# Performance work log

Measured on AMD Instinct MI355X. Metric: run time of the kernel, lower is better.

## Reference

```python
import jax, jax.numpy as jnp
import numpy as np

D = 768          # wav2vec2-base hidden size
H = 4            # cross-attn heads
HD = D // H
B = 8
N = 1024         # w2v sequence length (target length)
T = 2000         # raw CQCC frames
N_GAT = 3
NUM_CLASSES = 2


def _p(key, shape, scale=0.02):
    return jax.random.normal(key, shape, dtype=jnp.float32) * scale


def layer_norm(x, g, b, eps=1e-5):
    m = x.mean(-1, keepdims=True)
    v = x.var(-1, keepdims=True)
    return (x - m) * jax.lax.rsqrt(v + eps) * g + b


def gelu(x):
    return jax.nn.gelu(x, approximate=False)


def conv1d(x, w, b):
    # x [B,C,T], w [O,I,K], padding=1 (same)
    y = jax.lax.conv_general_dilated(x, w, (1,), [(1, 1)], dimension_numbers=('NCH', 'OIH', 'NCH'))
    return y + b[None, :, None]


def batchnorm(x, g, b, m, v, eps=1e-5):
    # eval-mode BatchNorm1d on [B,C,T]
    return (x - m[None, :, None]) * jax.lax.rsqrt(v[None, :, None] + eps) * g[None, :, None] + b[None, :, None]


def interp_linear(x, target_len):
    # torch F.interpolate(mode='linear', align_corners=False); x [B,T,D] -> [B,target_len,D]
    t_in = x.shape[1]
    pos = (jnp.arange(target_len, dtype=jnp.float32) + 0.5) * (t_in / target_len) - 0.5
    pos = jnp.clip(pos, 0.0, t_in - 1.0)
    lo = jnp.floor(pos).astype(jnp.int32)
    hi = jnp.minimum(lo + 1, t_in - 1)
    w = (pos - lo.astype(jnp.float32))[None, :, None]
    return x[:, lo] * (1.0 - w) + x[:, hi] * w


def mha(q, k, v, in_w, in_b, out_w, out_b):
    # torch nn.MultiheadAttention, batch_first=True
    bb, nq, _ = q.shape
    nk = k.shape[1]
    wq, wk, wv = in_w[:D], in_w[D:2 * D], in_w[2 * D:]
    bq, bk, bv = in_b[:D], in_b[D:2 * D], in_b[2 * D:]
    qh = (q @ wq.T + bq).reshape(bb, nq, H, HD).transpose(0, 2, 1, 3)
    kh = (k @ wk.T + bk).reshape(bb, nk, H, HD).transpose(0, 2, 1, 3)
    vh = (v @ wv.T + bv).reshape(bb, nk, H, HD).transpose(0, 2, 1, 3)
    scores = jnp.einsum('bhqd,bhkd->bhqk', qh, kh) * (1.0 / np.sqrt(HD))
    alpha = jax.nn.softmax(scores, axis=-1)
    o = jnp.einsum('bhqk,bhkd->bhqd', alpha, vh).transpose(0, 2, 1, 3).reshape(bb, nq, D)
    return o @ out_w.T + out_b


def graph_attn(x, fc_w, fc_b, a_w, a_b):
    # GAT score on concat([h_i, h_j]) decomposes additively: e_ij = a_i.h_i + a_j.h_j + b
    h = x @ fc_w.T + fc_b                      # [B,N,D]
    s_i = h @ a_w[:D]                          # [B,N]
    s_j = h @ a_w[D:]                          # [B,N]
    e = s_i[:, :, None] + s_j[:, None, :] + a_b  # [B,N,N]
    alpha = jax.nn.softmax(e, axis=-1)
    return jnp.einsum('bij,bjd->bid', alpha, h)


def _forward(w2v, cqcc, conv1_w, conv1_b, bn1_g, bn1_b, bn1_m, bn1_v,
             conv2_w, conv2_b, bn2_g, bn2_b, bn2_m, bn2_v, pos_embed,
             lnq_g, lnq_b, lnkv_g, lnkv_b,
             a1_in_w, a1_in_b, a1_out_w, a1_out_b,
             a2_in_w, a2_in_b, a2_out_w, a2_out_b,
             gat_fc_w, gat_fc_b, gat_a_w, gat_a_b, gln_g, gln_b,
             clf_w1, clf_b1, clf_w2, clf_b2):
    # CQCC conv stack
    x = gelu(batchnorm(conv1d(cqcc, conv1_w, conv1_b), bn1_g, bn1_b, bn1_m, bn1_v))
    x = gelu(batchnorm(conv1d(x, conv2_w, conv2_b), bn2_g, bn2_b, bn2_m, bn2_v))  # [B,D,T]
    cq = interp_linear(x.transpose(0, 2, 1), w2v.shape[1])  # [B,N,D]
    # shared positional encoding
    n = w2v.shape[1]
    w = w2v + pos_embed[:, :n]
    cq = cq + pos_embed[:, :n]
    # bidirectional cross attention (norm_q / norm_kv shared across directions)
    out1 = mha(layer_norm(cq, lnq_g, lnq_b), layer_norm(w, lnkv_g, lnkv_b),
               layer_norm(w, lnkv_g, lnkv_b), a1_in_w, a1_in_b, a1_out_w, a1_out_b)
    out2 = mha(layer_norm(w, lnq_g, lnq_b), layer_norm(cq, lnkv_g, lnkv_b),
               layer_norm(cq, lnkv_g, lnkv_b), a2_in_w, a2_in_b, a2_out_w, a2_out_b)
    x = out1 + out2
    # 3 residual graph-attention blocks
    for l in range(N_GAT):
        res = x
        x = graph_attn(x, gat_fc_w[l], gat_fc_b[l], gat_a_w[l], gat_a_b[l])
        x = layer_norm(x + res, gln_g[l], gln_b[l])
    pooled = x.mean(axis=1)
    h = gelu(pooled @ clf_w1.T + clf_b1)
    return h @ clf_w2.T + clf_b2


def setup_inputs():
    ks = iter(jax.random.split(jax.random.key(0), 64))
    inp = {}
    inp['w2v'] = jax.random.normal(next(ks), (B, N, D), dtype=jnp.float32)
    inp['cqcc'] = jax.random.normal(next(ks), (B, 20, T), dtype=jnp.float32)
    inp['conv1_w'] = _p(next(ks), (128, 20, 3)); inp['conv1_b'] = jnp.zeros((128,), jnp.float32)
    inp['bn1_g'] = jnp.ones((128,), jnp.float32); inp['bn1_b'] = jnp.zeros((128,), jnp.float32)
    inp['bn1_m'] = jnp.zeros((128,), jnp.float32); inp['bn1_v'] = jnp.ones((128,), jnp.float32)
    inp['conv2_w'] = _p(next(ks), (D, 128, 3)); inp['conv2_b'] = jnp.zeros((D,), jnp.float32)
    inp['bn2_g'] = jnp.ones((D,), jnp.float32); inp['bn2_b'] = jnp.zeros((D,), jnp.float32)
    inp['bn2_m'] = jnp.zeros((D,), jnp.float32); inp['bn2_v'] = jnp.ones((D,), jnp.float32)
    inp['pos_embed'] = _p(next(ks), (1, 2000, D), 1.0)
    inp['lnq_g'] = jnp.ones((D,), jnp.float32); inp['lnq_b'] = jnp.zeros((D,), jnp.float32)
    inp['lnkv_g'] = jnp.ones((D,), jnp.float32); inp['lnkv_b'] = jnp.zeros((D,), jnp.float32)
    inp['a1_in_w'] = _p(next(ks), (3 * D, D)); inp['a1_in_b'] = jnp.zeros((3 * D,), jnp.float32)
    inp['a1_out_w'] = _p(next(ks), (D, D)); inp['a1_out_b'] = jnp.zeros((D,), jnp.float32)
    inp['a2_in_w'] = _p(next(ks), (3 * D, D)); inp['a2_in_b'] = jnp.zeros((3 * D,), jnp.float32)
    inp['a2_out_w'] = _p(next(ks), (D, D)); inp['a2_out_b'] = jnp.zeros((D,), jnp.float32)
    inp['gat_fc_w'] = _p(next(ks), (N_GAT, D, D)); inp['gat_fc_b'] = jnp.zeros((N_GAT, D), jnp.float32)
    inp['gat_a_w'] = _p(next(ks), (N_GAT, 2 * D)); inp['gat_a_b'] = jnp.zeros((N_GAT,), jnp.float32)
    inp['gln_g'] = jnp.ones((N_GAT, D), jnp.float32); inp['gln_b'] = jnp.zeros((N_GAT, D), jnp.float32)
    inp['clf_w1'] = _p(next(ks), (128, D)); inp['clf_b1'] = jnp.zeros((128,), jnp.float32)
    inp['clf_w2'] = _p(next(ks), (NUM_CLASSES, 128)); inp['clf_b2'] = jnp.zeros((NUM_CLASSES,), jnp.float32)
    return inp


def reference(w2v, cqcc, conv1_w, conv1_b, bn1_g, bn1_b, bn1_m, bn1_v,
              conv2_w, conv2_b, bn2_g, bn2_b, bn2_m, bn2_v, pos_embed,
              lnq_g, lnq_b, lnkv_g, lnkv_b,
              a1_in_w, a1_in_b, a1_out_w, a1_out_b,
              a2_in_w, a2_in_b, a2_out_w, a2_out_b,
              gat_fc_w, gat_fc_b, gat_a_w, gat_a_b, gln_g, gln_b,
              clf_w1, clf_b1, clf_w2, clf_b2):
    return _forward(w2v, cqcc, conv1_w, conv1_b, bn1_g, bn1_b, bn1_m, bn1_v,
                    conv2_w, conv2_b, bn2_g, bn2_b, bn2_m, bn2_v, pos_embed,
                    lnq_g, lnq_b, lnkv_g, lnkv_b,
                    a1_in_w, a1_in_b, a1_out_w, a1_out_b,
                    a2_in_w, a2_in_b, a2_out_w, a2_out_b,
                    gat_fc_w, gat_fc_b, gat_a_w, gat_a_b, gln_g, gln_b,
                    clf_w1, clf_b1, clf_w2, clf_b2)
```

## Files before the change

kernel.cpp:

```cpp
#include <hip/hip_runtime.h>
#include <math.h>

#define DD 768
#define NH 4
#define HDIM 192
#define BBATCH 8
#define NSEQ 1024
#define TLEN 2000
#define SLOT 6291456
#define XROW 256256

typedef _Float16 h16;
typedef _Float16 half8v __attribute__((ext_vector_type(8)));
typedef _Float16 half4v __attribute__((ext_vector_type(4)));
typedef float f32x4 __attribute__((ext_vector_type(4)));

__device__ __forceinline__ float gelu_f(float x){
  return 0.5f * x * (1.0f + erff(x * 0.70710678118654752440f));
}
__device__ __forceinline__ float wave_sum(float v){
  #pragma unroll
  for (int off = 32; off; off >>= 1) v += __shfl_xor(v, off);
  return v;
}
__device__ __forceinline__ float wave_max(float v){
  #pragma unroll
  for (int off = 32; off; off >>= 1) v = fmaxf(v, __shfl_xor(v, off));
  return v;
}
__device__ __forceinline__ void gload16(const h16* g, h16* l){
  __builtin_amdgcn_global_load_lds(
      (const __attribute__((address_space(1))) void*)g,
      (__attribute__((address_space(3))) void*)l, 16, 0, 0);
}
__device__ __forceinline__ int xcd_remap(int orig, int nwg){
  int q = nwg >> 3, r = nwg & 7;
  int xcd = orig & 7, idx = orig >> 3;
  return (xcd < r ? xcd * (q + 1) : r * (q + 1) + (xcd - r) * q) + idx;
}

struct CastArgs {
  const float* s[5];
  h16* d[5];
  int cum[6];
};
__global__ __launch_bounds__(256) void k_cast5(CastArgs a, int total){
  int i = blockIdx.x * 256 + threadIdx.x;
  if (i >= total) return;
  int seg = 0;
  #pragma unroll
  for (int t = 1; t < 5; ++t) seg += (i >= a.cum[t]);
  int off = i - a.cum[seg];
  a.d[seg][off] = (h16)a.s[seg][off];
}

__global__ __launch_bounds__(256) void k_castc2(const float* __restrict__ s,
    h16* __restrict__ d){
  int i = blockIdx.x * 256 + threadIdx.x;
  if (i >= 294912) return;
  int oc = i / 384, rem = i % 384;
  int ic = rem / 3, kh = rem % 3;
  d[oc * 384 + kh * 128 + ic] = (h16)s[i];
}

__global__ __launch_bounds__(256) void k_conv1t(const float* __restrict__ cqcc,
    const float* __restrict__ w, const float* __restrict__ bias,
    const float* __restrict__ g, const float* __restrict__ be,
    const float* __restrict__ mm, const float* __restrict__ vv,
    h16* __restrict__ X){
  __shared__ float xs[20][258];
  __shared__ float wsm[32*60];
  const int t0 = blockIdx.x * 256;
  const int ocg = blockIdx.y, b = blockIdx.z;
  const int tid = threadIdx.x;
  for (int idx = tid; idx < 20*258; idx += 256){
    int ic = idx / 258, tt = idx % 258;
    int t = t0 + tt - 1;
    xs[ic][tt] = (t >= 0 && t < TLEN) ? cqcc[((size_t)b*20 + ic)*TLEN + t] : 0.f;
  }
  for (int idx = tid; idx < 32*60; idx += 256)
    wsm[idx] = w[ocg*32*60 + idx];
  __syncthreads();
  int t = t0 + tid;
  if (t >= TLEN) return;
  float acc[32] = {};
  for (int ic = 0; ic < 20; ++ic){
    float x0 = xs[ic][tid], x1v = xs[ic][tid+1], x2v = xs[ic][tid+2];
    #pragma unroll
    for (int oc = 0; oc < 32; ++oc){
      const float* wp = &wsm[(oc*20 + ic)*3];
      acc[oc] += wp[0]*x0 + wp[1]*x1v + wp[2]*x2v;
    }
  }
  h16* dst = X + (size_t)b*XROW + (size_t)(t+1)*128 + ocg*32;
  #pragma unroll 4
  for (int oc = 0; oc < 32; ++oc){
    int c = ocg*32 + oc;
    float s = rsqrtf(vv[c] + 1e-5f) * g[c];
    float val = (acc[oc] + bias[c] - mm[c]) * s + be[c];
    dst[oc] = (h16)gelu_f(val);
  }
  if (t == 0){
    h16* z = X + (size_t)b*XROW + ocg*32;
    #pragma unroll
    for (int oc = 0; oc < 32; ++oc) z[oc] = (h16)0.f;
  }
  if (t == TLEN-1){
    h16* z = X + (size_t)b*XROW + (size_t)2001*128 + ocg*32;
    #pragma unroll
    for (int oc = 0; oc < 32; ++oc) z[oc] = (h16)0.f;
  }
}

__global__ void k_bnprep(const float* __restrict__ cb, const float* __restrict__ g,
    const float* __restrict__ be, const float* __restrict__ m,
    const float* __restrict__ v, float* __restrict__ sc, float* __restrict__ off){
  int i = blockIdx.x * 256 + threadIdx.x;
  if (i >= DD) return;
  float s = g[i] * rsqrtf(v[i] + 1e-5f);
  sc[i] = s;
  off[i] = (cb[i] - m[i]) * s + be[i];
}

__global__ __launch_bounds__(256) void k_interp_ln(const h16* __restrict__ x2,
    const float* __restrict__ pe,
    const float* __restrict__ g1, const float* __restrict__ b1, h16* __restrict__ o1,
    const float* __restrict__ g2, const float* __restrict__ b2, h16* __restrict__ o2){
  __shared__ float ss[4], sqq[4];
  int row = blockIdx.x, tid = threadIdx.x;
  int b = row >> 10, i = row & 1023;
  float p = (i + 0.5f) * ((float)TLEN / (float)NSEQ) - 0.5f;
  p = fminf(fmaxf(p, 0.f), (float)(TLEN - 1));
  int lo = (int)floorf(p);
  int hi = min(lo + 1, TLEN - 1);
  float w = p - (float)lo;
  const h16* blo = x2 + ((size_t)b * TLEN + lo) * DD;
  const h16* bhi = x2 + ((size_t)b * TLEN + hi) * DD;
  const float* per = pe + (size_t)i * DD;
  float v[3]; float s = 0.f, sq = 0.f;
  #pragma unroll
  for (int j = 0; j < 3; ++j){
    int d = j * 256 + tid;
    float x = (float)blo[d] * (1.f - w) + (float)bhi[d] * w + per[d];
    v[j] = x; s += x; sq += x * x;
  }
  s = wave_sum(s); sq = wave_sum(sq);
  int wv = tid >> 6;
  if ((tid & 63) == 0){ ss[wv] = s; sqq[wv] = sq; }
  __syncthreads();
  s  = ss[0] + ss[1] + ss[2] + ss[3];
  sq = sqq[0] + sqq[1] + sqq[2] + sqq[3];
  float mean = s * (1.f / DD);
  float var  = sq * (1.f / DD) - mean * mean;
  float r = rsqrtf(var + 1e-5f);
  #pragma unroll
  for (int j = 0; j < 3; ++j){
    int d = j * 256 + tid;
    float xn = (v[j] - mean) * r;
    o1[(size_t)row * DD + d] = (h16)(xn * g1[d] + b1[d]);
    o2[(size_t)row * DD + d] = (h16)(xn * g2[d] + b2[d]);
  }
}

__global__ __launch_bounds__(256) void k_addpos_ln(const float* __restrict__ xin,
    const float* __restrict__ pe,
    const float* __restrict__ g1, const float* __restrict__ b1, h16* __restrict__ o1,
    const float* __restrict__ g2, const float* __restrict__ b2, h16* __restrict__ o2){
  __shared__ float ss[4], sqq[4];
  int row = blockIdx.x, tid = threadIdx.x;
  int i = row & 1023;
  const float* ip = xin + (size_t)row * DD;
  const float* per = pe + (size_t)i * DD;
  float v[3]; float s = 0.f, sq = 0.f;
  #pragma unroll
  for (int j = 0; j < 3; ++j){
    int d = j * 256 + tid;
    float x = ip[d] + per[d];
    v[j] = x; s += x; sq += x * x;
  }
  s = wave_sum(s); sq = wave_sum(sq);
  int wv = tid >> 6;
  if ((tid & 63) == 0){ ss[wv] = s; sqq[wv] = sq; }
  __syncthreads();
  s  = ss[0] + ss[1] + ss[2] + ss[3];
  sq = sqq[0] + sqq[1] + sqq[2] + sqq[3];
  float mean = s * (1.f / DD);
  float var  = sq * (1.f / DD) - mean * mean;
  float r = rsqrtf(var + 1e-5f);
  #pragma unroll
  for (int j = 0; j < 3; ++j){
    int d = j * 256 + tid;
    float xn = (v[j] - mean) * r;
    o1[(size_t)row * DD + d] = (h16)(xn * g1[d] + b1[d]);
    o2[(size_t)row * DD + d] = (h16)(xn * g2[d] + b2[d]);
  }
}

__global__ __launch_bounds__(256) void k_lnH(const h16* __restrict__ in,
    const float* __restrict__ ctx, const float* __restrict__ g,
    const float* __restrict__ be, h16* __restrict__ out){
  __shared__ float ss[4], sqq[4];
  int row = blockIdx.x, tid = threadIdx.x;
  const h16* ip = in + (size_t)row * DD;
  int b = row >> 10;
  float v[3]; float s = 0.f, sq = 0.f;
  #pragma unroll
  for (int j = 0; j < 3; ++j){
    int d = j * 256 + tid;
    float x = (float)ip[d] + ctx[b * DD + d];
    v[j] = x; s += x; sq += x * x;
  }
  s = wave_sum(s); sq = wave_sum(sq);
  int w = tid >> 6;
  if ((tid & 63) == 0){ ss[w] = s; sqq[w] = sq; }
  __syncthreads();
  s  = ss[0] + ss[1] + ss[2] + ss[3];
  sq = sqq[0] + sqq[1] + sqq[2] + sqq[3];
  float mean = s * (1.f / DD);
  float var  = sq * (1.f / DD) - mean * mean;
  float r = rsqrtf(var + 1e-5f);
  #pragma unroll
  for (int j = 0; j < 3; ++j){
    int d = j * 256 + tid;
    out[(size_t)row * DD + d] = (h16)((v[j] - mean) * r * g[d] + be[d]);
  }
}

__global__ __launch_bounds__(256) void k_addh(const h16* __restrict__ a,
    const h16* __restrict__ b, h16* __restrict__ o, int n8){
  int i = blockIdx.x * 256 + threadIdx.x;
  if (i < n8){
    half8v x = ((const half8v*)a)[i];
    half8v y = ((const half8v*)b)[i];
    ((half8v*)o)[i] = x + y;
  }
}

#define GEMM_MAINLOOP(Abase, lda, Wbase, ldw, Kdim)                          \
  auto stage = [&](int buf, int kt){                                         \
    _Pragma("unroll")                                                        \
    for (int i = 0; i < 4; ++i){                                             \
      int p = i*256 + tid; int row = p >> 3; int ch = (p & 7) ^ (row & 7);   \
      gload16(Abase + (size_t)(m0+row)*lda + kt + ch*8, &Als[buf][p*8]);     \
    }                                                                        \
    _Pragma("unroll")                                                        \
    for (int i = 0; i < 4; ++i){                                             \
      int p = i*256 + tid; int row = p >> 3; int ch = (p & 7) ^ (row & 7);   \
      gload16(Wbase + (size_t)(n0+row)*ldw + kt + ch*8, &Bls[buf][p*8]);     \
    }                                                                        \
  };                                                                         \
  stage(0, 0);                                                               \
  const int nk = Kdim >> 6;                                                  \
  for (int t = 0; t < nk; ++t){                                              \
    const int cur = t & 1;                                                   \
    if (t + 1 < nk){                                                         \
      stage(cur ^ 1, (t + 1) << 6);                                          \
      asm volatile("s_waitcnt vmcnt(8)" ::: "memory");                       \
    } else {                                                                 \
      asm volatile("s_waitcnt vmcnt(0)" ::: "memory");                       \
    }                                                                        \
    __builtin_amdgcn_s_barrier();                                            \
    __builtin_amdgcn_sched_barrier(0);                                       \
    __builtin_amdgcn_s_setprio(1);                                           \
    _Pragma("unroll")                                                        \
    for (int kk = 0; kk < 2; ++kk){                                          \
      half8v af[4], bf[4];                                                   \
      _Pragma("unroll")                                                      \
      for (int mi = 0; mi < 4; ++mi){                                        \
        int row = wr*64 + mi*16 + lr;                                        \
        int chp = (kk*4 + lg) ^ (row & 7);                                   \
        af[mi] = *(const half8v*)&Als[cur][row*64 + chp*8];                  \
      }                                                                      \
      _Pragma("unroll")                                                      \
      for (int ni = 0; ni < 4; ++ni){                                        \
        int row = wc*64 + ni*16 + lr;                                        \
        int chp = (kk*4 + lg) ^ (row & 7);                                   \
        bf[ni] = *(const half8v*)&Bls[cur][row*64 + chp*8];                  \
      }                                                                      \
      _Pragma("unroll")                                                      \
      for (int mi = 0; mi < 4; ++mi)                                         \
        _Pragma("unroll")                                                    \
        for (int ni = 0; ni < 4; ++ni)                                       \
          acc[mi][ni] = __builtin_amdgcn_mfma_f32_16x16x32_f16(              \
              af[mi], bf[ni], acc[mi][ni], 0, 0, 0);                         \
    }                                                                        \
    __builtin_amdgcn_s_setprio(0);                                           \
    asm volatile("s_waitcnt lgkmcnt(0)" ::: "memory");                       \
    __builtin_amdgcn_sched_barrier(0);                                       \
    __builtin_amdgcn_s_barrier();                                            \
  }

__global__ __launch_bounds__(256) void k_gemm_h(
    const h16* __restrict__ A, const h16* __restrict__ W,
    int lda, int ldw, int ldc, int K,
    const float* __restrict__ bias,
    h16* __restrict__ outh,
    const float* __restrict__ rdw, float* __restrict__ rdpart)
{
  __shared__ h16 Als[2][128*64];
  __shared__ h16 Bls[2][128*64];
  const int tid = threadIdx.x;
  const int gx = gridDim.x, gy = gridDim.y;
  const int wg = xcd_remap(blockIdx.x + gx * blockIdx.y, gx * gy);
  const int nidx = wg % gx;
  const int n0 = nidx * 128, m0 = (wg / gx) * 128;
  const int lane = tid & 63, wid = tid >> 6;
  const int wr = wid >> 1, wc = wid & 1;
  const int lr = lane & 15, lg = lane >> 4;
  f32x4 acc[4][4] = {};
  GEMM_MAINLOOP(A, lda, W, ldw, K)
  float rd[4][4] = {};
  #pragma unroll
  for (int mi = 0; mi < 4; ++mi){
    #pragma unroll
    for (int ni = 0; ni < 4; ++ni){
      int col = n0 + wc*64 + ni*16 + lr;
      int rowb = m0 + wr*64 + mi*16 + lg*4;
      float cb = bias[col];
      float aw = rdw ? rdw[col] : 0.f;
      #pragma unroll
      for (int r = 0; r < 4; ++r){
        size_t idx = (size_t)(rowb + r) * ldc + col;
        float v = acc[mi][ni][r] + cb;
        outh[idx] = (h16)v;
        if (rdw) rd[mi][r] += v * aw;
      }
    }
  }
  if (rdw){
    #pragma unroll
    for (int mi = 0; mi < 4; ++mi){
      #pragma unroll
      for (int r = 0; r < 4; ++r){
        float p = rd[mi][r];
        #pragma unroll
        for (int o = 1; o < 16; o <<= 1) p += __shfl_xor(p, o);
        if (lr == 0){
          int row = m0 + wr*64 + mi*16 + lg*4 + r;
          rdpart[(size_t)row * 12 + nidx*2 + wc] = p;
        }
      }
    }
  }
}

__global__ __launch_bounds__(256) void k_gemmop(
    const h16* __restrict__ A0, const h16* __restrict__ A1,
    const h16* __restrict__ W0, const h16* __restrict__ W1,
    const float* __restrict__ bb0, const float* __restrict__ bb1,
    h16* __restrict__ C0, h16* __restrict__ C1)
{
  __shared__ h16 Als[2][128*64];
  __shared__ h16 Bls[2][128*64];
  const int tid = threadIdx.x;
  const int gx = gridDim.x, gy = gridDim.y;
  const int nwg = gx * gy * 2;
  const int wg = xcd_remap(blockIdx.x + gx*(blockIdx.y + gy*blockIdx.z), nwg);
  const int n0 = (wg % gx) * 128;
  const int m0 = ((wg / gx) % gy) * 128;
  const int bz = wg / (gx * gy);
  const h16* A = bz ? A1 : A0;
  const h16* W = bz ? W1 : W0;
  const float* bias = bz ? bb1 : bb0;
  h16* C = bz ? C1 : C0;
  const int lane = tid & 63, wid = tid >> 6;
  const int wr = wid >> 1, wc = wid & 1;
  const int lr = lane & 15, lg = lane >> 4;
  f32x4 acc[4][4] = {};
  GEMM_MAINLOOP(A, DD, W, DD, DD)
  #pragma unroll
  for (int mi = 0; mi < 4; ++mi){
    #pragma unroll
    for (int ni = 0; ni < 4; ++ni){
      int col = n0 + wc*64 + ni*16 + lr;
      int rowb = m0 + wr*64 + mi*16 + lg*4;
      float cb = bias[col];
      #pragma unroll
      for (int r = 0; r < 4; ++r)
        C[(size_t)(rowb + r) * DD + col] = (h16)(acc[mi][ni][r] + cb);
    }
  }
}

__global__ __launch_bounds__(256) void k_conv2g(
    const h16* __restrict__ X, const h16* __restrict__ W,
    const float* __restrict__ sc, const float* __restrict__ off,
    h16* __restrict__ out)
{
  __shared__ h16 Als[2][128*64];
  __shared__ h16 Bls[2][128*64];
  const int tid = threadIdx.x;
  const int gx = gridDim.x, gy = gridDim.y;
  const int wg = xcd_remap(blockIdx.x + gx * blockIdx.y, gx * gy);
  const int n0 = (wg % gx) * 128, m0 = (wg / gx) * 128;
  const int lane = tid & 63, wid = tid >> 6;
  const int wr = wid >> 1, wc = wid & 1;
  const int lr = lane & 15, lg = lane >> 4;
  f32x4 acc[4][4] = {};
  auto stage = [&](int buf, int kt){
    #pragma unroll
    for (int i = 0; i < 4; ++i){
      int p = i*256 + tid; int row = p >> 3; int ch = (p & 7) ^ (row & 7);
      int rm = m0 + row, b = rm >> 11, t = rm & 2047;
      gload16(X + (size_t)b*XROW + (size_t)t*128 + kt + ch*8, &Als[buf][p*8]);
    }
    #pragma unroll
    for (int i = 0; i < 4; ++i){
      int p = i*256 + tid; int row = p >> 3; int ch = (p & 7) ^ (row & 7);
      gload16(W + (size_t)(n0+row)*384 + kt + ch*8, &Bls[buf][p*8]);
    }
  };
  stage(0, 0);
  const int nk = 6;
  for (int t = 0; t < nk; ++t){
    const int cur = t & 1;
    if (t + 1 < nk){
      stage(cur ^ 1, (t + 1) << 6);
      asm volatile("s_waitcnt vmcnt(8)" ::: "memory");
    } else {
      asm volatile("s_waitcnt vmcnt(0)" ::: "memory");
    }
    __builtin_amdgcn_s_barrier();
    __builtin_amdgcn_sched_barrier(0);
    __builtin_amdgcn_s_setprio(1);
    #pragma unroll
    for (int kk = 0; kk < 2; ++kk){
      half8v af[4], bf[4];
      #pragma unroll
      for (int mi = 0; mi < 4; ++mi){
        int row = wr*64 + mi*16 + lr;
        int chp = (kk*4 + lg) ^ (row & 7);
        af[mi] = *(const half8v*)&Als[cur][row*64 + chp*8];
      }
      #pragma unroll
      for (int ni = 0; ni < 4; ++ni){
        int row = wc*64 + ni*16 + lr;
        int chp = (kk*4 + lg) ^ (row & 7);
        bf[ni] = *(const half8v*)&Bls[cur][row*64 + chp*8];
      }
      #pragma unroll
      for (int mi = 0; mi < 4; ++mi)
        #pragma unroll
        for (int ni = 0; ni < 4; ++ni)
          acc[mi][ni] = __builtin_amdgcn_mfma_f32_16x16x32_f16(
              af[mi], bf[ni], acc[mi][ni], 0, 0, 0);
    }
    __builtin_amdgcn_s_setprio(0);
    asm volatile("s_waitcnt lgkmcnt(0)" ::: "memory");
    __builtin_amdgcn_sched_barrier(0);
    __builtin_amdgcn_s_barrier();
  }
  #pragma unroll
  for (int mi = 0; mi < 4; ++mi){
    #pragma unroll
    for (int ni = 0; ni < 4; ++ni){
      int col = n0 + wc*64 + ni*16 + lr;
      int rowb = m0 + wr*64 + mi*16 + lg*4;
      #pragma unroll
      for (int r = 0; r < 4; ++r){
        int rm = rowb + r, b = rm >> 11, t = rm & 2047;
        if (t < TLEN){
          float v = acc[mi][ni][r] * sc[col] + off[col];
          out[((size_t)b*TLEN + t)*DD + col] = (h16)gelu_f(v);
        }
      }
    }
  }
}

__global__ __launch_bounds__(256) void k_gemm6(
    const h16* __restrict__ Lall, const h16* __restrict__ w6,
    const float* __restrict__ b1, const float* __restrict__ b2,
    h16* __restrict__ qkv6)
{
  __shared__ h16 Als[2][128*64];
  __shared__ h16 Bls[2][128*64];
  const int tid = threadIdx.x;
  const int gx = gridDim.x, gy = gridDim.y;
  const int nwg = gx * gy * 6;
  const int wg = xcd_remap(blockIdx.x + gx*(blockIdx.y + gy*blockIdx.z), nwg);
  const int n0 = (wg % gx) * 128;
  const int m0 = ((wg / gx) % gy) * 128;
  const int bz = wg / (gx * gy);
  const int aidx = (1468 >> (2*bz)) & 3;
  const h16* A = Lall + (size_t)aidx * SLOT;
  const h16* W = w6 + (size_t)bz * 589824;
  const float* bias = (bz < 3 ? b1 + bz*DD : b2 + (bz-3)*DD);
  h16* C = qkv6 + (size_t)bz * SLOT;
  const int lane = tid & 63, wid = tid >> 6;
  const int wr = wid >> 1, wc = wid & 1;
  const int lr = lane & 15, lg = lane >> 4;
  f32x4 acc[4][4] = {};
  GEMM_MAINLOOP(A, DD, W, DD, DD)
  #pragma unroll
  for (int mi = 0; mi < 4; ++mi){
    #pragma unroll
    for (int ni = 0; ni < 4; ++ni){
      int col = n0 + wc*64 + ni*16 + lr;
      int rowb = m0 + wr*64 + mi*16 + lg*4;
      float cb = bias[col];
      #pragma unroll
      for (int r = 0; r < 4; ++r)
        C[(size_t)(rowb + r) * DD + col] = (h16)(acc[mi][ni][r] + cb);
    }
  }
}

__global__ __launch_bounds__(256) void k_trV(const h16* __restrict__ V0,
    const h16* __restrict__ V1, h16* __restrict__ VT0, h16* __restrict__ VT1){
  __shared__ h16 tile[64*64];
  const int zz = blockIdx.z;
  const int which = zz >> 5, bh = zz & 31;
  const int b = bh >> 2, h = bh & 3;
  const h16* Vh = which ? V1 : V0;
  h16* VT = which ? VT1 : VT0;
  const int q0 = blockIdx.x * 64, d0 = blockIdx.y * 64;
  const int t = threadIdx.x;
  {
    int qq = t >> 2, ds = (t & 3) * 16;
    const h16* src = Vh + ((size_t)b*NSEQ + q0 + qq)*DD + h*HDIM + d0 + ds;
    half8v v0 = *(const half8v*)src;
    half8v v1 = *(const half8v*)(src + 8);
    int c0 = (ds >> 3) ^ (qq & 7), c1 = ((ds >> 3) + 1) ^ (qq & 7);
    *(half8v*)&tile[qq*64 + c0*8] = v0;
    *(half8v*)&tile[qq*64 + c1*8] = v1;
  }
  __syncthreads();
  {
    int dd = t >> 2, qs = (t & 3) * 16;
    half8v o0, o1;
    #pragma unroll
    for (int j = 0; j < 8; ++j){
      int q = qs + j, q2 = qs + 8 + j;
      o0[j] = tile[q*64  + (((dd>>3) ^ (q&7))*8)  + (dd & 7)];
      o1[j] = tile[q2*64 + (((dd>>3) ^ (q2&7))*8) + (dd & 7)];
    }
    h16* dst = VT + (size_t)bh*HDIM*NSEQ + (size_t)(d0+dd)*NSEQ + q0 + qs;
    *(half8v*)dst = o0;
    *(half8v*)(dst + 8) = o1;
  }
}

__global__ __launch_bounds__(256, 3) void k_flash(
    const h16* __restrict__ Q0, const h16* __restrict__ K0,
    const h16* __restrict__ T0, h16* __restrict__ O0,
    const h16* __restrict__ Q1, const h16* __restrict__ K1,
    const h16* __restrict__ T1, h16* __restrict__ O1){
  __shared__ h16 Ks[2][32*192];
  __shared__ h16 Vs[2][192*32];
  __shared__ h16 Ps[4][16*32];
  const int tid = threadIdx.x;
  const int bh = blockIdx.x, qt = blockIdx.y, which = blockIdx.z;
  const int b = bh >> 2, h = bh & 3;
  const int q0 = qt * 64;
  const h16* Qp = which ? Q1 : Q0;
  const h16* Kp = which ? K1 : K0;
  const h16* VTp = which ? T1 : T0;
  h16* Op = which ? O1 : O0;
  const h16* Qg = Qp + (size_t)b*NSEQ*DD + h*HDIM;
  const h16* Kg = Kp + (size_t)b*NSEQ*DD + h*HDIM;
  const h16* Vg = VTp + (size_t)bh*HDIM*NSEQ;
  const int lane = tid & 63, wid = tid >> 6;
  const int lr = lane & 15, lg = lane >> 4;
  const float SC2 = 0.07216878364870322f * 1.4426950408889634f;
  half8v qf[6];
  {
    int qrow = q0 + wid*16 + lr;
    const h16 qs2 = (h16)SC2;
    #pragma unroll
    for (int ks = 0; ks < 6; ++ks){
      half8v qv = *(const half8v*)(Qg + (size_t)qrow*DD + ks*32 + lg*8);
      #pragma unroll
      for (int j = 0; j < 8; ++j) qv[j] = qv[j] * qs2;
      qf[ks] = qv;
    }
  }
  auto stageK = [&](int buf, int k0){
    #pragma unroll
    for (int i = 0; i < 3; ++i){
      int p = i*256 + tid;
      int row = p / 24, chp = p % 24;
      int ch = chp ^ (row & 7);
      gload16(Kg + (size_t)(k0+row)*DD + ch*8, &Ks[buf][p*8]);
    }
  };
  auto stageV = [&](int buf, int k0){
    #pragma unroll
    for (int i = 0; i < 3; ++i){
      int p = i*256 + tid;
      int row = p >> 2, chp = p & 3;
      int ch = chp ^ ((row >> 1) & 3);
      gload16(Vg + (size_t)row*NSEQ + k0 + ch*8, &Vs[buf][p*8]);
    }
  };
  stageK(0, 0); stageV(0, 0);
  f32x4 oacc[12] = {};
  f32x4 osum = {0.f, 0.f, 0.f, 0.f};
  float m2[4] = {-1e30f, -1e30f, -1e30f, -1e30f};
  half8v vone;
  #pragma unroll
  for (int j = 0; j < 8; ++j) vone[j] = (h16)1.f;
  for (int kt = 0; kt < 32; ++kt){
    const int cur = kt & 1;
    if (kt + 1 < 32){
      stageK(cur^1, (kt+1)*32); stageV(cur^1, (kt+1)*32);
      asm volatile("s_waitcnt vmcnt(6)" ::: "memory");
    } else {
      asm volatile("s_waitcnt vmcnt(0)" ::: "memory");
    }
    __builtin_amdgcn_s_barrier();
    __builtin_amdgcn_sched_barrier(0);
    f32x4 sacc[2] = {};
    __builtin_amdgcn_s_setprio(1);
    #pragma unroll
    for (int ks = 0; ks < 6; ++ks){
      #pragma unroll
      for (int t = 0; t < 2; ++t){
        int krow = t*16 + lr;
        int ch = (ks*4 + lg) ^ (krow & 7);
        half8v kf = *(const half8v*)&Ks[cur][krow*192 + ch*8];
        sacc[t] = __builtin_amdgcn_mfma_f32_16x16x32_f16(qf[ks], kf, sacc[t], 0, 0, 0);
      }
    }
    __builtin_amdgcn_s_setprio(0);
    float lmaxr[4];
    #pragma unroll
    for (int r = 0; r < 4; ++r) lmaxr[r] = fmaxf(sacc[0][r], sacc[1][r]);
    bool flag = false;
    #pragma unroll
    for (int r = 0; r < 4; ++r) flag |= (lmaxr[r] > m2[r] + 14.f);
    if (__ballot(flag)){
      float c[4];
      #pragma unroll
      for (int r = 0; r < 4; ++r){
        float mt = lmaxr[r];
        #pragma unroll
        for (int off = 1; off < 16; off <<= 1) mt = fmaxf(mt, __shfl_xor(mt, off));
        if (mt > m2[r]){ c[r] = exp2f(m2[r] - mt); m2[r] = mt; }
        else c[r] = 1.f;
      }
      #pragma unroll
      for (int dt = 0; dt < 12; ++dt){
        f32x4 o = oacc[dt];
        o[0] *= c[0]; o[1] *= c[1]; o[2] *= c[2]; o[3] *= c[3];
        oacc[dt] = o;
      }
      osum[0] *= c[0]; osum[1] *= c[1]; osum[2] *= c[2]; osum[3] *= c[3];
    }
    #pragma unroll
    for (int t = 0; t < 2; ++t){
      #pragma unroll
      for (int r = 0; r < 4; ++r){
        float p = exp2f(sacc[t][r] - m2[r]);
        int q = lg*4 + r, key = t*16 + lr;
        int ch = (t*2 + (lr>>3)) ^ ((q>>1) & 3);
        Ps[wid][q*32 + ch*8 + (key & 7)] = (h16)p;
      }
    }
    asm volatile("s_waitcnt lgkmcnt(0)" ::: "memory");
    __builtin_amdgcn_sched_barrier(0);
    {
      int pch = lg ^ ((lr >> 1) & 3);
      half8v pf = *(const half8v*)&Ps[wid][lr*32 + pch*8];
      __builtin_amdgcn_s_setprio(1);
      #pragma unroll
      for (int dt = 0; dt < 12; ++dt){
        int drow = dt*16 + lr;
        int vch = lg ^ ((drow >> 1) & 3);
        half8v vf = *(const half8v*)&Vs[cur][drow*32 + vch*8];
        oacc[dt] = __builtin_amdgcn_mfma_f32_16x16x32_f16(pf, vf, oacc[dt], 0, 0, 0);
      }
      osum = __builtin_amdgcn_mfma_f32_16x16x32_f16(pf, vone, osum, 0, 0, 0);
      __builtin_amdgcn_s_setprio(0);
    }
    asm volatile("s_waitcnt lgkmcnt(0)" ::: "memory");
    __builtin_amdgcn_sched_barrier(0);
    __builtin_amdgcn_s_barrier();
  }
  float inv[4];
  #pragma unroll
  for (int r = 0; r < 4; ++r) inv[r] = 1.0f / osum[r];
  h16* Og = Op + (size_t)b*NSEQ*DD + h*HDIM;
  #pragma unroll
  for (int dt = 0; dt < 12; ++dt){
    #pragma unroll
    for (int r = 0; r < 4; ++r){
      int q = q0 + wid*16 + lg*4 + r;
      Og[(size_t)q*DD + dt*16 + lr] = (h16)(oacc[dt][r] * inv[r]);
    }
  }
}

__global__ __launch_bounds__(256) void k_ctxs(const float* __restrict__ rdpart,
    const h16* __restrict__ h, float* __restrict__ part){
  __shared__ float red[4];
  __shared__ float al[64];
  const int tid = threadIdx.x;
  const int b = blockIdx.y, pc = blockIdx.z;
  float v[4]; float mx = -1e30f;
  #pragma unroll
  for (int j = 0; j < 4; ++j){
    int i = j * 256 + tid;
    const float* p = rdpart + (size_t)(b * NSEQ + i) * 12;
    float s = 0.f;
    #pragma unroll
    for (int k = 0; k < 12; ++k) s += p[k];
    v[j] = s; mx = fmaxf(mx, s);
  }
  mx = wave_max(mx);
  if ((tid & 63) == 0) red[tid >> 6] = mx;
  __syncthreads();
  mx = fmaxf(fmaxf(red[0], red[1]), fmaxf(red[2], red[3]));
  __syncthreads();
  float s = 0.f;
  #pragma unroll
  for (int j = 0; j < 4; ++j){ v[j] = __expf(v[j] - mx); s += v[j]; }
  s = wave_sum(s);
  if ((tid & 63) == 0) red[tid >> 6] = s;
  __syncthreads();
  s = red[0] + red[1] + red[2] + red[3];
  float inv = 1.0f / s;
  #pragma unroll
  for (int j = 0; j < 4; ++j){
    int i = j * 256 + tid;
    int rel = i - pc * 64;
    if (rel >= 0 && rel < 64) al[rel] = v[j] * inv;
  }
  __syncthreads();
  int d = blockIdx.x * 256 + tid;
  float acc = 0.f;
  const h16* hp = h + ((size_t)b * NSEQ + pc * 64) * DD + d;
  #pragma unroll 4
  for (int j = 0; j < 64; ++j) acc += al[j] * (float)hp[(size_t)j * DD];
  part[(size_t)(b * 16 + pc) * DD + d] = acc;
}

__global__ __launch_bounds__(256) void k_ctx2(const float* __restrict__ part,
    float scale, float* __restrict__ ctx){
  int d = blockIdx.x * 256 + threadIdx.x;
  int b = blockIdx.y;
  if (d >= DD) return;
  float acc = 0.f;
  #pragma unroll
  for (int p = 0; p < 16; ++p) acc += part[(size_t)(b * 16 + p) * DD + d];
  ctx[b * DD + d] = acc * scale;
}

__global__ __launch_bounds__(256) void k_pool1(const h16* __restrict__ x,
    float* __restrict__ part){
  int d = blockIdx.x * 256 + threadIdx.x;
  int b = blockIdx.y, pc = blockIdx.z;
  if (d >= DD) return;
  float acc = 0.f;
  const h16* xp = x + ((size_t)b * NSEQ + pc * 64) * DD + d;
  #pragma unroll 4
  for (int j = 0; j < 64; ++j) acc += (float)xp[(size_t)j * DD];
  part[(size_t)(b * 16 + pc) * DD + d] = acc;
}

__global__ __launch_bounds__(128) void k_clf(const float* __restrict__ pooled,
    const float* __restrict__ w1, const float* __restrict__ b1,
    const float* __restrict__ w2, const float* __restrict__ b2,
    float* __restrict__ out){
  __shared__ float pl[DD];
  __shared__ float h1[128];
  int b = blockIdx.x, tid = threadIdx.x;
  #pragma unroll
  for (int j = 0; j < 6; ++j) pl[j * 128 + tid] = pooled[b * DD + j * 128 + tid];
  __syncthreads();
  float acc = b1[tid];
  const float* wp = w1 + (size_t)tid * DD;
  for (int d = 0; d < DD; ++d) acc += pl[d] * wp[d];
  h1[tid] = gelu_f(acc);
  __syncthreads();
  if (tid < 2){
    float o = b2[tid];
    const float* w2p = w2 + tid * 128;
    for (int c = 0; c < 128; ++c) o += h1[c] * w2p[c];
    out[b * 2 + tid] = o;
  }
}

extern "C" void kernel_launch(void* const* d_in, const int* in_sizes, int n_in,
                              void* d_out, int out_size, void* d_ws, size_t ws_size,
                              hipStream_t stream){
  (void)in_sizes; (void)n_in; (void)out_size;
  const float* w2v      = (const float*)d_in[0];
  const float* cqcc     = (const float*)d_in[1];
  const float* conv1_w  = (const float*)d_in[2];
  const float* conv1_b  = (const float*)d_in[3];
  const float* bn1_g    = (const float*)d_in[4];
  const float* bn1_b    = (const float*)d_in[5];
  const float* bn1_m    = (const float*)d_in[6];
  const float* bn1_v    = (const float*)d_in[7];
  const float* conv2_w  = (const float*)d_in[8];
  const float* conv2_b  = (const float*)d_in[9];
  const float* bn2_g    = (const float*)d_in[10];
  const float* bn2_b    = (const float*)d_in[11];
  const float* bn2_m    = (const float*)d_in[12];
  const float* bn2_v    = (const float*)d_in[13];
  const float* pos_embed= (const float*)d_in[14];
  const float* lnq_g    = (const float*)d_in[15];
  const float* lnq_b    = (const float*)d_in[16];
  const float* lnkv_g   = (const float*)d_in[17];
  const float* lnkv_b   = (const float*)d_in[18];
  const float* a1_in_w  = (const float*)d_in[19];
  const float* a1_in_b  = (const float*)d_in[20];
  const float* a1_out_w = (const float*)d_in[21];
  const float* a1_out_b = (const float*)d_in[22];
  const float* a2_in_w  = (const float*)d_in[23];
  const float* a2_in_b  = (const float*)d_in[24];
  const float* a2_out_w = (const float*)d_in[25];
  const float* a2_out_b = (const float*)d_in[26];
  const float* gat_fc_w = (const float*)d_in[27];
  const float* gat_fc_b = (const float*)d_in[28];
  const float* gat_a_w  = (const float*)d_in[29];
  const float* gln_g    = (const float*)d_in[31];
  const float* gln_b    = (const float*)d_in[32];
  const float* clf_w1   = (const float*)d_in[33];
  const float* clf_b1   = (const float*)d_in[34];
  const float* clf_w2   = (const float*)d_in[35];
  const float* clf_b2   = (const float*)d_in[36];

  char* wsp = (char*)d_ws;
  auto F = [&](size_t bytes){ char* p = wsp; wsp += (bytes + 255) & ~(size_t)255; return p; };
  h16* xh      = (h16*)F(12582912);
  h16* Lall    = (h16*)F(4*12582912);
  h16* qkv6    = (h16*)F(6*12582912);
  h16* VT      = (h16*)F(12582912);
  h16* VT2     = (h16*)F(12582912);
  h16* o1h     = (h16*)F(12582912);
  h16* o2h     = (h16*)F(12582912);
  h16* w6      = (h16*)F(2*3538944);
  h16* w_a1out = (h16*)F(1179648);
  h16* w_a2out = (h16*)F(1179648);
  h16* w_gat   = (h16*)F(3538944);
  h16* w_c2    = (h16*)F(589824);
  float* scb   = (float*)F(3072);
  float* offb  = (float*)F(3072);
  float* ctxb  = (float*)F(24576);
  float* pooled= (float*)F(24576);
  float* partb = (float*)F(393216);
  float* partc = (float*)F(393216);
  if ((size_t)(wsp - (char*)d_ws) > ws_size) return;

  h16* X   = Lall;
  h16* x2h = qkv6;
  h16* hh  = qkv6;

  const int NR = BBATCH * NSEQ;

  {
    CastArgs ca;
    ca.s[0]=a1_in_w;  ca.d[0]=w6;            int n0=1769472;
    ca.s[1]=a2_in_w;  ca.d[1]=w6+1769472;    int n1=1769472;
    ca.s[2]=a1_out_w; ca.d[2]=w_a1out;       int n2=589824;
    ca.s[3]=a2_out_w; ca.d[3]=w_a2out;       int n3=589824;
    ca.s[4]=gat_fc_w; ca.d[4]=w_gat;         int n4=1769472;
    ca.cum[0]=0; ca.cum[1]=n0; ca.cum[2]=n0+n1; ca.cum[3]=n0+n1+n2;
    ca.cum[4]=n0+n1+n2+n3; ca.cum[5]=n0+n1+n2+n3+n4;
    int total = ca.cum[5];
    k_cast5<<<(total+255)/256, 256, 0, stream>>>(ca, total);
  }
  k_castc2<<<(294912+255)/256, 256, 0, stream>>>(conv2_w, w_c2);
  k_bnprep<<<3, 256, 0, stream>>>(conv2_b, bn2_g, bn2_b, bn2_m, bn2_v, scb, offb);

  k_conv1t<<<dim3(8, 4, BBATCH), 256, 0, stream>>>(cqcc, conv1_w, conv1_b,
      bn1_g, bn1_b, bn1_m, bn1_v, X);
  k_conv2g<<<dim3(6, 128), 256, 0, stream>>>(X, w_c2, scb, offb, x2h);

  k_interp_ln<<<NR, 256, 0, stream>>>(x2h, pos_embed,
      lnq_g, lnq_b, Lall, lnkv_g, lnkv_b, Lall + SLOT);
  k_addpos_ln<<<NR, 256, 0, stream>>>(w2v, pos_embed,
      lnq_g, lnq_b, Lall + 2*SLOT, lnkv_g, lnkv_b, Lall + 3*SLOT);

  k_gemm6<<<dim3(6, 64, 6), 256, 0, stream>>>(Lall, w6, a1_in_b, a2_in_b, qkv6);

  k_trV<<<dim3(16, 3, 64), 256, 0, stream>>>(qkv6 + 2*(size_t)SLOT,
      qkv6 + 5*(size_t)SLOT, VT, VT2);
  k_flash<<<dim3(32, 16, 2), 256, 0, stream>>>(
      qkv6, qkv6 + (size_t)SLOT, VT, qkv6,
      qkv6 + 3*(size_t)SLOT, qkv6 + 4*(size_t)SLOT, VT2,
      qkv6 + 3*(size_t)SLOT);
  k_gemmop<<<dim3(6, 64, 2), 256, 0, stream>>>(
      qkv6, qkv6 + 3*(size_t)SLOT, w_a1out, w_a2out,
      a1_out_b, a2_out_b, o1h, o2h);
  k_addh<<<(NR*DD/8 + 255)/256, 256, 0, stream>>>(o1h, o2h, xh, NR*DD/8);

  for (int l = 0; l < 3; ++l){
    k_gemm_h<<<dim3(6, 64), 256, 0, stream>>>(xh, w_gat + (size_t)l*589824,
        DD, DD, DD, DD, gat_fc_b + l*DD, hh, gat_a_w + l*2*DD + DD, partb);
    k_ctxs<<<dim3(3, BBATCH, 16), 256, 0, stream>>>(partb, hh, partc);
    k_ctx2<<<dim3(3, BBATCH), 256, 0, stream>>>(partc, 1.0f, ctxb);
    k_lnH<<<NR, 256, 0, stream>>>(xh, ctxb, gln_g + l*DD, gln_b + l*DD, xh);
  }

  k_pool1<<<dim3(3, BBATCH, 16), 256, 0, stream>>>(xh, partb);
  k_ctx2<<<dim3(3, BBATCH), 256, 0, stream>>>(partb, 1.0f/NSEQ, pooled);
  k_clf<<<BBATCH, 128, 0, stream>>>(pooled, clf_w1, clf_b1, clf_w2, clf_b2,
                                    (float*)d_out);
}
```

Before: 525.6 us.

## Process two query tiles per flash-attention block to reuse staged K/V

```diff
diff --git a/kernel.cpp b/kernel.cpp
--- a/kernel.cpp
+++ b/kernel.cpp
@@ -541,7 +541,7 @@
   }
 }
 
-__global__ __launch_bounds__(256, 3) void k_flash(
+__global__ __launch_bounds__(256, 2) void k_flash(
     const h16* __restrict__ Q0, const h16* __restrict__ K0,
     const h16* __restrict__ T0, h16* __restrict__ O0,
     const h16* __restrict__ Q1, const h16* __restrict__ K1,
@@ -552,7 +552,7 @@
   const int tid = threadIdx.x;
   const int bh = blockIdx.x, qt = blockIdx.y, which = blockIdx.z;
   const int b = bh >> 2, h = bh & 3;
-  const int q0 = qt * 64;
+  const int q0a = qt * 64, q0b = (qt + 8) * 64;
   const h16* Qp = which ? Q1 : Q0;
   const h16* Kp = which ? K1 : K0;
   const h16* VTp = which ? T1 : T0;
@@ -563,16 +563,17 @@
   const int lane = tid & 63, wid = tid >> 6;
   const int lr = lane & 15, lg = lane >> 4;
   const float SC2 = 0.07216878364870322f * 1.4426950408889634f;
-  half8v qf[6];
+  half8v qfa[6], qfb[6];
   {
-    int qrow = q0 + wid*16 + lr;
     const h16 qs2 = (h16)SC2;
+    int qra = q0a + wid*16 + lr, qrb = q0b + wid*16 + lr;
     #pragma unroll
     for (int ks = 0; ks < 6; ++ks){
-      half8v qv = *(const half8v*)(Qg + (size_t)qrow*DD + ks*32 + lg*8);
-      #pragma unroll
-      for (int j = 0; j < 8; ++j) qv[j] = qv[j] * qs2;
-      qf[ks] = qv;
+      half8v va = *(const half8v*)(Qg + (size_t)qra*DD + ks*32 + lg*8);
+      half8v vb = *(const half8v*)(Qg + (size_t)qrb*DD + ks*32 + lg*8);
+      #pragma unroll
+      for (int j = 0; j < 8; ++j){ va[j] = va[j] * qs2; vb[j] = vb[j] * qs2; }
+      qfa[ks] = va; qfb[ks] = vb;
     }
   }
   auto stageK = [&](int buf, int k0){
@@ -594,12 +595,83 @@
     }
   };
   stageK(0, 0); stageV(0, 0);
-  f32x4 oacc[12] = {};
-  f32x4 osum = {0.f, 0.f, 0.f, 0.f};
-  float m2[4] = {-1e30f, -1e30f, -1e30f, -1e30f};
+  f32x4 oacca[12] = {}, oaccb[12] = {};
+  f32x4 osuma = {0.f, 0.f, 0.f, 0.f}, osumb = {0.f, 0.f, 0.f, 0.f};
+  float m2a[4] = {-1e30f, -1e30f, -1e30f, -1e30f};
+  float m2b[4] = {-1e30f, -1e30f, -1e30f, -1e30f};
   half8v vone;
   #pragma unroll
   for (int j = 0; j < 8; ++j) vone[j] = (h16)1.f;
+
+  auto process = [&](half8v (&qf)[6], f32x4 (&oacc)[12], f32x4 &osum,
+                     float (&m2)[4], int cur){
+    f32x4 sacc[2] = {};
+    __builtin_amdgcn_s_setprio(1);
+    #pragma unroll
+    for (int ks = 0; ks < 6; ++ks){
+      #pragma unroll
+      for (int t = 0; t < 2; ++t){
+        int krow = t*16 + lr;
+        int ch = (ks*4 + lg) ^ (krow & 7);
+        half8v kf = *(const half8v*)&Ks[cur][krow*192 + ch*8];
+        sacc[t] = __builtin_amdgcn_mfma_f32_16x16x32_f16(qf[ks], kf, sacc[t], 0, 0, 0);
+      }
+    }
+    __builtin_amdgcn_s_setprio(0);
+    float lmaxr[4];
+    #pragma unroll
+    for (int r = 0; r < 4; ++r) lmaxr[r] = fmaxf(sacc[0][r], sacc[1][r]);
+    bool flag = false;
+    #pragma unroll
+    for (int r = 0; r < 4; ++r) flag |= (lmaxr[r] > m2[r] + 14.f);
+    if (__ballot(flag)){
+      float c[4];
+      #pragma unroll
+      for (int r = 0; r < 4; ++r){
+        float mt = lmaxr[r];
+        #pragma unroll
+        for (int off = 1; off < 16; off <<= 1) mt = fmaxf(mt, __shfl_xor(mt, off));
+        if (mt > m2[r]){ c[r] = exp2f(m2[r] - mt); m2[r] = mt; }
+        else c[r] = 1.f;
+      }
+      #pragma unroll
+      for (int dt = 0; dt < 12; ++dt){
+        f32x4 o = oacc[dt];
+        o[0] *= c[0]; o[1] *= c[1]; o[2] *= c[2]; o[3] *= c[3];
+        oacc[dt] = o;
+      }
+      osum[0] *= c[0]; osum[1] *= c[1]; osum[2] *= c[2]; osum[3] *= c[3];
+    }
+    #pragma unroll
+    for (int t = 0; t < 2; ++t){
+      #pragma unroll
+      for (int r = 0; r < 4; ++r){
+        float p = exp2f(sacc[t][r] - m2[r]);
+        int q = lg*4 + r, key = t*16 + lr;
+        int ch = (t*2 + (lr>>3)) ^ ((q>>1) & 3);
+        Ps[wid][q*32 + ch*8 + (key & 7)] = (h16)p;
+      }
+    }
+    asm volatile("s_waitcnt lgkmcnt(0)" ::: "memory");
+    __builtin_amdgcn_sched_barrier(0);
+    {
+      int pch = lg ^ ((lr >> 1) & 3);
+      half8v pf = *(const half8v*)&Ps[wid][lr*32 + pch*8];
+      __builtin_amdgcn_s_setprio(1);
+      #pragma unroll
+      for (int dt = 0; dt < 12; ++dt){
+        int drow = dt*16 + lr;
+        int vch = lg ^ ((drow >> 1) & 3);
+        half8v vf = *(const half8v*)&Vs[cur][drow*32 + vch*8];
+        oacc[dt] = __builtin_amdgcn_mfma_f32_16x16x32_f16(pf, vf, oacc[dt], 0, 0, 0);
+      }
+      osum = __builtin_amdgcn_mfma_f32_16x16x32_f16(pf, vone, osum, 0, 0, 0);
+      __builtin_amdgcn_s_setprio(0);
+    }
+    asm volatile("s_waitcnt lgkmcnt(0)" ::: "memory");
+    __builtin_amdgcn_sched_barrier(0);
+  };
+
   for (int kt = 0; kt < 32; ++kt){
     const int cur = kt & 1;
     if (kt + 1 < 32){
@@ -610,83 +682,32 @@
     }
     __builtin_amdgcn_s_barrier();
     __builtin_amdgcn_sched_barrier(0);
-    f32x4 sacc[2] = {};
-    __builtin_amdgcn_s_setprio(1);
-    #pragma unroll
-    for (int ks = 0; ks < 6; ++ks){
-      #pragma unroll
-      for (int t = 0; t < 2; ++t){
-        int krow = t*16 + lr;
-        int ch = (ks*4 + lg) ^ (krow & 7);
-        half8v kf = *(const half8v*)&Ks[cur][krow*192 + ch*8];
-        sacc[t] = __builtin_amdgcn_mfma_f32_16x16x32_f16(qf[ks], kf, sacc[t], 0, 0, 0);
-      }
-    }
-    __builtin_amdgcn_s_setprio(0);
-    float lmaxr[4];
-    #pragma unroll
-    for (int r = 0; r < 4; ++r) lmaxr[r] = fmaxf(sacc[0][r], sacc[1][r]);
-    bool flag = false;
-    #pragma unroll
-    for (int r = 0; r < 4; ++r) flag |= (lmaxr[r] > m2[r] + 14.f);
-    if (__ballot(flag)){
-      float c[4];
+    process(qfa, oacca, osuma, m2a, cur);
+    process(qfb, oaccb, osumb, m2b, cur);
+    __builtin_amdgcn_s_barrier();
+  }
+  {
+    float inv[4];
+    #pragma unroll
+    for (int r = 0; r < 4; ++r) inv[r] = 1.0f / osuma[r];
+    h16* Og = Op + (size_t)b*NSEQ*DD + h*HDIM;
+    #pragma unroll
+    for (int dt = 0; dt < 12; ++dt){
       #pragma unroll
       for (int r = 0; r < 4; ++r){
-        float mt = lmaxr[r];
-        #pragma unroll
-        for (int off = 1; off < 16; off <<= 1) mt = fmaxf(mt, __shfl_xor(mt, off));
-        if (mt > m2[r]){ c[r] = exp2f(m2[r] - mt); m2[r] = mt; }
-        else c[r] = 1.f;
-      }
-      #pragma unroll
-      for (int dt = 0; dt < 12; ++dt){
-        f32x4 o = oacc[dt];
-        o[0] *= c[0]; o[1] *= c[1]; o[2] *= c[2]; o[3] *= c[3];
-        oacc[dt] = o;
-      }
-      osum[0] *= c[0]; osum[1] *= c[1]; osum[2] *= c[2]; osum[3] *= c[3];
-    }
-    #pragma unroll
-    for (int t = 0; t < 2; ++t){
+        int q = q0a + wid*16 + lg*4 + r;
+        Og[(size_t)q*DD + dt*16 + lr] = (h16)(oacca[dt][r] * inv[r]);
+      }
+    }
+    #pragma unroll
+    for (int r = 0; r < 4; ++r) inv[r] = 1.0f / osumb[r];
+    #pragma unroll
+    for (int dt = 0; dt < 12; ++dt){
       #pragma unroll
       for (int r = 0; r < 4; ++r){
-        float p = exp2f(sacc[t][r] - m2[r]);
-        int q = lg*4 + r, key = t*16 + lr;
-        int ch = (t*2 + (lr>>3)) ^ ((q>>1) & 3);
-        Ps[wid][q*32 + ch*8 + (key & 7)] = (h16)p;
-      }
-    }
-    asm volatile("s_waitcnt lgkmcnt(0)" ::: "memory");
-    __builtin_amdgcn_sched_barrier(0);
-    {
-      int pch = lg ^ ((lr >> 1) & 3);
-      half8v pf = *(const half8v*)&Ps[wid][lr*32 + pch*8];
-      __builtin_amdgcn_s_setprio(1);
-      #pragma unroll
-      for (int dt = 0; dt < 12; ++dt){
-        int drow = dt*16 + lr;
-        int vch = lg ^ ((drow >> 1) & 3);
-        half8v vf = *(const half8v*)&Vs[cur][drow*32 + vch*8];
-        oacc[dt] = __builtin_amdgcn_mfma_f32_16x16x32_f16(pf, vf, oacc[dt], 0, 0, 0);
-      }
-      osum = __builtin_amdgcn_mfma_f32_16x16x32_f16(pf, vone, osum, 0, 0, 0);
-      __builtin_amdgcn_s_setprio(0);
-    }
-    asm volatile("s_waitcnt lgkmcnt(0)" ::: "memory");
-    __builtin_amdgcn_sched_barrier(0);
-    __builtin_amdgcn_s_barrier();
-  }
-  float inv[4];
-  #pragma unroll
-  for (int r = 0; r < 4; ++r) inv[r] = 1.0f / osum[r];
-  h16* Og = Op + (size_t)b*NSEQ*DD + h*HDIM;
-  #pragma unroll
-  for (int dt = 0; dt < 12; ++dt){
-    #pragma unroll
-    for (int r = 0; r < 4; ++r){
-      int q = q0 + wid*16 + lg*4 + r;
-      Og[(size_t)q*DD + dt*16 + lr] = (h16)(oacc[dt][r] * inv[r]);
+        int q = q0b + wid*16 + lg*4 + r;
+        Og[(size_t)q*DD + dt*16 + lr] = (h16)(oaccb[dt][r] * inv[r]);
+      }
     }
   }
 }
@@ -878,7 +899,7 @@
 
   k_trV<<<dim3(16, 3, 64), 256, 0, stream>>>(qkv6 + 2*(size_t)SLOT,
       qkv6 + 5*(size_t)SLOT, VT, VT2);
-  k_flash<<<dim3(32, 16, 2), 256, 0, stream>>>(
+  k_flash<<<dim3(32, 8, 2), 256, 0, stream>>>(
       qkv6, qkv6 + (size_t)SLOT, VT, qkv6,
       qkv6 + 3*(size_t)SLOT, qkv6 + 4*(size_t)SLOT, VT2,
       qkv6 + 3*(size_t)SLOT);
```

New measurement: 520.5 us, median of 2. Within noise of the previous version (-1.0%).
